# Kernel optimization log

Measured on AMD Instinct MI355X. Metric: run time of the kernel, lower is better.

The kernel has to match this reference:

```python
import jax, jax.numpy as jnp
import numpy as np

N_HEAD = 16

def setup_inputs() -> dict:
    key = jax.random.key(0)
    ks = jax.random.split(key, 5)
    C = 1024
    x = jax.random.normal(ks[0], (2, 2048, C), dtype=jnp.float32)
    W_qkv = jax.random.normal(ks[1], (C, 3 * C), dtype=jnp.float32) * (C ** -0.5)
    b_qkv = jnp.zeros((3 * C,), dtype=jnp.float32)
    W_proj = jax.random.normal(ks[2], (C, C), dtype=jnp.float32) * (C ** -0.5)
    b_proj = jnp.zeros((C,), dtype=jnp.float32)
    return {"x": x, "W_qkv": W_qkv, "b_qkv": b_qkv, "W_proj": W_proj, "b_proj": b_proj}

def reference(x, W_qkv, b_qkv, W_proj, b_proj):
    B, T, C = x.shape
    H = N_HEAD
    D = C // H
    scale = D ** -0.5
    qkv = x @ W_qkv + b_qkv                      # [B,T,3C]
    q, k, v = jnp.split(qkv, 3, axis=-1)
    # [B,T,C] -> [B,H,T,D]
    q = q.reshape(B, T, H, D).transpose(0, 2, 1, 3)
    k = k.reshape(B, T, H, D).transpose(0, 2, 1, 3)
    v = v.reshape(B, T, H, D).transpose(0, 2, 1, 3)
    attn = jnp.einsum('bhqd,bhkd->bhqk', q, k) * scale   # [B,H,T,T]
    causal = jnp.tril(jnp.ones((T, T), dtype=bool))
    attn = jnp.where(causal, attn, -jnp.inf)
    attn = jax.nn.softmax(attn, axis=-1)
    y = jnp.einsum('bhqk,bhkd->bhqd', attn, v)           # [B,H,T,D]
    y = y.transpose(0, 2, 1, 3).reshape(B, T, C)
    return y @ W_proj + b_proj
```

## Files before the change

### kernel.cpp

```cpp
#include <hip/hip_runtime.h>

typedef __attribute__((ext_vector_type(8))) _Float16 h8;
typedef __attribute__((ext_vector_type(4))) _Float16 h4;
typedef __attribute__((ext_vector_type(4))) float f4;

#define QKSCALE 0.18033688011112042f

__device__ __forceinline__ void gload16(const void* g, void* l) {
  __builtin_amdgcn_global_load_lds((const __attribute__((address_space(1))) void*)g,
                                   (__attribute__((address_space(3))) void*)l, 16, 0, 0);
}

__global__ __launch_bounds__(256) void cast_f16_kernel(const float* __restrict__ in,
                                                       _Float16* __restrict__ out, int n) {
  int i = (blockIdx.x * 256 + threadIdx.x) * 8;
  if (i >= n) return;
  const float4* p = (const float4*)(in + i);
  float4 a = p[0], b = p[1];
  h8 v;
  v[0] = (_Float16)a.x; v[1] = (_Float16)a.y; v[2] = (_Float16)a.z; v[3] = (_Float16)a.w;
  v[4] = (_Float16)b.x; v[5] = (_Float16)b.y; v[6] = (_Float16)b.z; v[7] = (_Float16)b.w;
  *(h8*)(out + i) = v;
}

__global__ __launch_bounds__(256) void transp_cast_kernel(const float* __restrict__ W,
                                                          _Float16* __restrict__ Wt, int K, int N) {
  __shared__ _Float16 tile[64][72];
  int k0 = blockIdx.y * 64, n0 = blockIdx.x * 64;
  int t = threadIdx.x;
#pragma unroll
  for (int i = 0; i < 16; ++i) {
    int idx = i * 256 + t;
    int kr = idx >> 6, nc = idx & 63;
    tile[kr][nc] = (_Float16)W[(size_t)(k0 + kr) * N + n0 + nc];
  }
  __syncthreads();
#pragma unroll
  for (int i = 0; i < 2; ++i) {
    int idx = i * 256 + t;
    int nr = idx >> 3, kc = (idx & 7) * 8;
    h8 v;
#pragma unroll
    for (int j = 0; j < 8; ++j) v[j] = tile[kc + j][nr];
    *(h8*)&Wt[(size_t)(n0 + nr) * K + k0 + kc] = v;
  }
}

template <int MODE>
__global__ __launch_bounds__(256) void gemm_f16(const _Float16* __restrict__ A,
                                                const _Float16* __restrict__ Bt,
                                                const float* __restrict__ bias,
                                                float* __restrict__ outF,
                                                _Float16* __restrict__ oQ,
                                                _Float16* __restrict__ oK,
                                                _Float16* __restrict__ oV,
                                                int M, int N, int K) {
  __shared__ _Float16 As[128 * 64];
  __shared__ _Float16 Bs[128 * 64];
  const int m0 = blockIdx.y * 128, n0 = blockIdx.x * 128;
  const int tid = threadIdx.x;
  const int wave = tid >> 6, lane = tid & 63;
  const int wr = (wave >> 1) * 64, wc = (wave & 1) * 64;
  const int lrow = lane & 15, g = lane >> 4;

  const int row_ = tid >> 3, c_ = tid & 7;

  f4 acc[4][4];
  const f4 z4 = {0.f, 0.f, 0.f, 0.f};
#pragma unroll
  for (int m = 0; m < 4; ++m)
#pragma unroll
    for (int n = 0; n < 4; ++n) acc[m][n] = z4;

  for (int k0 = 0; k0 < K; k0 += 64) {
#pragma unroll
    for (int i = 0; i < 4; ++i) {
      int row = i * 32 + row_;
      int cs = (c_ ^ (row & 7)) * 8;
      int ldst = (i * 256 + tid) * 8;
      gload16(&A[(size_t)(m0 + row) * K + k0 + cs], &As[ldst]);
      gload16(&Bt[(size_t)(n0 + row) * K + k0 + cs], &Bs[ldst]);
    }
    __syncthreads();
#pragma unroll
    for (int ss = 0; ss < 2; ++ss) {
      h8 af[4], bf[4];
#pragma unroll
      for (int m = 0; m < 4; ++m) {
        int row = wr + m * 16 + lrow;
        af[m] = *(const h8*)&As[row * 64 + (((ss * 4 + g) ^ (row & 7)) * 8)];
      }
#pragma unroll
      for (int n = 0; n < 4; ++n) {
        int row = wc + n * 16 + lrow;
        bf[n] = *(const h8*)&Bs[row * 64 + (((ss * 4 + g) ^ (row & 7)) * 8)];
      }
      __builtin_amdgcn_s_setprio(1);
#pragma unroll
      for (int m = 0; m < 4; ++m)
#pragma unroll
        for (int n = 0; n < 4; ++n)
          acc[m][n] = __builtin_amdgcn_mfma_f32_16x16x32_f16(af[m], bf[n], acc[m][n], 0, 0, 0);
      __builtin_amdgcn_s_setprio(0);
    }
    __syncthreads();
  }

#pragma unroll
  for (int n = 0; n < 4; ++n) {
    const int gcol = n0 + wc + n * 16 + lrow;
    const float bv = bias ? bias[gcol] : 0.f;
    if (MODE == 1 && (gcol >> 10) == 2) {
      const int c1 = gcol & 1023;
      const int hh = c1 >> 6, d = c1 & 63;
#pragma unroll
      for (int m = 0; m < 4; ++m) {
        const int grow = m0 + wr + m * 16 + g * 4;
        const int b = grow >> 11, t = grow & 2047;
        h4 pv;
#pragma unroll
        for (int r = 0; r < 4; ++r) pv[r] = (_Float16)(acc[m][n][r] + bv);
        *(h4*)&oV[(((size_t)(b * 16 + hh)) * 64 + d) * 2048 + t] = pv;
      }
    } else {
#pragma unroll
      for (int m = 0; m < 4; ++m) {
#pragma unroll
        for (int r = 0; r < 4; ++r) {
          const int grow = m0 + wr + m * 16 + g * 4 + r;
          float v = acc[m][n][r] + bv;
          if (MODE == 0) {
            outF[(size_t)grow * N + gcol] = v;
          } else {
            int part = gcol >> 10;
            int c1 = gcol & 1023;
            int hh = c1 >> 6, d = c1 & 63;
            int b = grow >> 11, t = grow & 2047;
            int bh = b * 16 + hh;
            if (part == 0)
              oQ[((size_t)bh * 2048 + t) * 64 + d] = (_Float16)(v * QKSCALE);
            else
              oK[((size_t)bh * 2048 + t) * 64 + d] = (_Float16)v;
          }
        }
      }
    }
  }
}

__global__ __launch_bounds__(256) void attn_kernel(const _Float16* __restrict__ Qg,
                                                   const _Float16* __restrict__ Kg,
                                                   const _Float16* __restrict__ Vtg,
                                                   _Float16* __restrict__ Og) {
  __shared__ _Float16 slab[4][32][72];
  __shared__ float mlds[2][4][32];

  const int idx = blockIdx.x;
  const int bh = (idx & 7) | (((idx >> 3) & 3) << 3);
  const int pi = idx >> 5;

  const int wave = threadIdx.x >> 6, lane = threadIdx.x & 63;
  const int lrow = lane & 15, g = lane >> 4;
  const int b = bh >> 4, h = bh & 15;
  const _Float16* Q = Qg + (size_t)bh * 2048 * 64;
  const _Float16* K = Kg + (size_t)bh * 2048 * 64;
  const _Float16* Vt = Vtg + (size_t)bh * 64 * 2048;
  _Float16(*pw)[72] = slab[wave];
  const f4 z4 = {0.f, 0.f, 0.f, 0.f};

  for (int half = 0; half < 2; ++half) {
    const int qt2 = half == 0 ? 63 - pi : pi;
    const int q0 = qt2 * 32;

    h8 aq[2][2];
#pragma unroll
    for (int mt = 0; mt < 2; ++mt)
#pragma unroll
      for (int ss = 0; ss < 2; ++ss)
        aq[mt][ss] = *(const h8*)&Q[(q0 + mt * 16 + lrow) * 64 + ss * 32 + g * 8];

    f4 o[2][4];
#pragma unroll
    for (int mt = 0; mt < 2; ++mt)
#pragma unroll
      for (int dt = 0; dt < 4; ++dt) o[mt][dt] = z4;
    float mrow[2][4], lpart[2][4];
#pragma unroll
    for (int mt = 0; mt < 2; ++mt)
#pragma unroll
      for (int r = 0; r < 4; ++r) { mrow[mt][r] = -1e30f; lpart[mt][r] = 0.f; }

    const int NT = (qt2 >> 1) + 1;

    for (int it = wave; it < NT; it += 4) {
      const int kv0 = it * 64;
      h8 kf[4][2];
#pragma unroll
      for (int ct = 0; ct < 4; ++ct)
#pragma unroll
        for (int ss = 0; ss < 2; ++ss)
          kf[ct][ss] = *(const h8*)&K[(kv0 + ct * 16 + lrow) * 64 + ss * 32 + g * 8];

      f4 s[2][4];
#pragma unroll
      for (int mt = 0; mt < 2; ++mt)
#pragma unroll
        for (int ct = 0; ct < 4; ++ct) s[mt][ct] = z4;
#pragma unroll
      for (int ss = 0; ss < 2; ++ss)
#pragma unroll
        for (int mt = 0; mt < 2; ++mt)
#pragma unroll
          for (int ct = 0; ct < 4; ++ct)
            s[mt][ct] = __builtin_amdgcn_mfma_f32_16x16x32_f16(aq[mt][ss], kf[ct][ss], s[mt][ct], 0, 0, 0);

      h8 vf[4][2];
#pragma unroll
      for (int dt = 0; dt < 4; ++dt)
#pragma unroll
        for (int ss = 0; ss < 2; ++ss)
          vf[dt][ss] = *(const h8*)&Vt[(size_t)(dt * 16 + lrow) * 2048 + kv0 + ss * 32 + g * 8];

      if (it == NT - 1) {
#pragma unroll
        for (int mt = 0; mt < 2; ++mt)
#pragma unroll
          for (int ct = 0; ct < 4; ++ct)
#pragma unroll
            for (int r = 0; r < 4; ++r)
              if (kv0 + ct * 16 + lrow > q0 + mt * 16 + g * 4 + r) s[mt][ct][r] = -1e30f;
      }

      float pm[2][4];
      bool need = false;
#pragma unroll
      for (int mt = 0; mt < 2; ++mt)
#pragma unroll
        for (int r = 0; r < 4; ++r) {
          pm[mt][r] = fmaxf(fmaxf(s[mt][0][r], s[mt][1][r]), fmaxf(s[mt][2][r], s[mt][3][r]));
          need = need || (pm[mt][r] > mrow[mt][r] + 8.f);
        }
      if (__any(need)) {
#pragma unroll
        for (int mt = 0; mt < 2; ++mt)
#pragma unroll
          for (int r = 0; r < 4; ++r) {
            float m = pm[mt][r];
            m = fmaxf(m, __shfl_xor(m, 1));
            m = fmaxf(m, __shfl_xor(m, 2));
            m = fmaxf(m, __shfl_xor(m, 4));
            m = fmaxf(m, __shfl_xor(m, 8));
            float mn = fmaxf(mrow[mt][r], m);
            float fr = __builtin_amdgcn_exp2f(mrow[mt][r] - mn);
            mrow[mt][r] = mn;
            lpart[mt][r] *= fr;
#pragma unroll
            for (int dt = 0; dt < 4; ++dt) o[mt][dt][r] *= fr;
          }
      }
#pragma unroll
      for (int mt = 0; mt < 2; ++mt)
#pragma unroll
        for (int r = 0; r < 4; ++r) {
          float ps = 0.f;
#pragma unroll
          for (int ct = 0; ct < 4; ++ct) {
            float p = __builtin_amdgcn_exp2f(s[mt][ct][r] - mrow[mt][r]);
            ps += p;
            pw[mt * 16 + g * 4 + r][ct * 16 + lrow] = (_Float16)p;
          }
          lpart[mt][r] += ps;
        }

      h8 ap[2][2];
#pragma unroll
      for (int mt = 0; mt < 2; ++mt)
#pragma unroll
        for (int ss = 0; ss < 2; ++ss)
          ap[mt][ss] = *(const h8*)&pw[mt * 16 + lrow][ss * 32 + g * 8];

#pragma unroll
      for (int ss = 0; ss < 2; ++ss)
#pragma unroll
        for (int mt = 0; mt < 2; ++mt)
#pragma unroll
          for (int dt = 0; dt < 4; ++dt)
            o[mt][dt] = __builtin_amdgcn_mfma_f32_16x16x32_f16(ap[mt][ss], vf[dt][ss], o[mt][dt], 0, 0, 0);
    }

#pragma unroll
    for (int mt = 0; mt < 2; ++mt)
#pragma unroll
      for (int r = 0; r < 4; ++r) {
        float l = lpart[mt][r];
        l += __shfl_xor(l, 1);
        l += __shfl_xor(l, 2);
        l += __shfl_xor(l, 4);
        l += __shfl_xor(l, 8);
        lpart[mt][r] = l;
      }

    if (lrow == 0) {
#pragma unroll
      for (int mt = 0; mt < 2; ++mt)
#pragma unroll
        for (int r = 0; r < 4; ++r) {
          mlds[0][wave][mt * 16 + g * 4 + r] = mrow[mt][r];
          mlds[1][wave][mt * 16 + g * 4 + r] = lpart[mt][r];
        }
    }
#pragma unroll
    for (int mt = 0; mt < 2; ++mt)
#pragma unroll
      for (int r = 0; r < 4; ++r) {
        float inv = lpart[mt][r] > 0.f ? 1.f / lpart[mt][r] : 0.f;
#pragma unroll
        for (int dt = 0; dt < 4; ++dt)
          pw[mt * 16 + g * 4 + r][dt * 16 + lrow] = (_Float16)(o[mt][dt][r] * inv);
      }
    __syncthreads();

    {
      const int ql = threadIdx.x >> 3;
      const int d0 = (threadIdx.x & 7) * 8;
      float m0 = mlds[0][0][ql], m1 = mlds[0][1][ql], m2 = mlds[0][2][ql], m3 = mlds[0][3][ql];
      float M = fmaxf(fmaxf(m0, m1), fmaxf(m2, m3));
      float f0 = __builtin_amdgcn_exp2f(m0 - M) * mlds[1][0][ql];
      float f1 = __builtin_amdgcn_exp2f(m1 - M) * mlds[1][1][ql];
      float f2 = __builtin_amdgcn_exp2f(m2 - M) * mlds[1][2][ql];
      float f3 = __builtin_amdgcn_exp2f(m3 - M) * mlds[1][3][ql];
      float inv = 1.f / (f0 + f1 + f2 + f3);
      h8 o0 = *(const h8*)&slab[0][ql][d0];
      h8 o1 = *(const h8*)&slab[1][ql][d0];
      h8 o2 = *(const h8*)&slab[2][ql][d0];
      h8 o3 = *(const h8*)&slab[3][ql][d0];
      h8 outv;
#pragma unroll
      for (int j = 0; j < 8; ++j) {
        float v = f0 * (float)o0[j] + f1 * (float)o1[j] + f2 * (float)o2[j] + f3 * (float)o3[j];
        outv[j] = (_Float16)(v * inv);
      }
      *(h8*)&Og[((size_t)b * 2048 + q0 + ql) * 1024 + h * 64 + d0] = outv;
    }
    if (half == 0) __syncthreads();
  }
}

extern "C" void kernel_launch(void* const* d_in, const int* in_sizes, int n_in,
                              void* d_out, int out_size, void* d_ws, size_t ws_size,
                              hipStream_t stream) {
  const float* x = (const float*)d_in[0];
  const float* Wqkv = (const float*)d_in[1];
  const float* bqkv = (const float*)d_in[2];
  const float* Wproj = (const float*)d_in[3];
  const float* bproj = (const float*)d_in[4];
  float* out = (float*)d_out;

  char* ws = (char*)d_ws;
  const size_t MB = 1u << 20;
  _Float16* xh     = (_Float16*)(ws + 0 * MB);
  _Float16* wqkvt  = (_Float16*)(ws + 8 * MB);
  _Float16* wprojt = (_Float16*)(ws + 14 * MB);
  _Float16* qh     = (_Float16*)(ws + 16 * MB);
  _Float16* kh     = (_Float16*)(ws + 24 * MB);
  _Float16* vth    = (_Float16*)(ws + 32 * MB);
  _Float16* oh     = (_Float16*)(ws + 40 * MB);

  cast_f16_kernel<<<2048, 256, 0, stream>>>(x, xh, 4194304);
  transp_cast_kernel<<<dim3(48, 16), 256, 0, stream>>>(Wqkv, wqkvt, 1024, 3072);
  transp_cast_kernel<<<dim3(16, 16), 256, 0, stream>>>(Wproj, wprojt, 1024, 1024);

  gemm_f16<1><<<dim3(24, 32), 256, 0, stream>>>(xh, wqkvt, bqkv, nullptr, qh, kh, vth,
                                                4096, 3072, 1024);
  attn_kernel<<<dim3(1024), 256, 0, stream>>>(qh, kh, vth, oh);
  gemm_f16<0><<<dim3(8, 32), 256, 0, stream>>>(oh, wprojt, bproj, out, nullptr, nullptr, nullptr,
                                               4096, 1024, 1024);
}
```

Baseline: 151.8 us.

## Rewrite attention inner loop with 32x32x16 MFMA and register-resident P

Switches the attention kernel from 16x16x32 MFMA tiles to 32x32x16 tiles and computes S transposed (K as the A operand, Q as B), so each lane owns one query column. Softmax row max and sum then need only a single cross-half shuffle. P is packed to fp16 in registers and rearranged with lane swaps to feed the PV MFMA directly, removing the per-tile LDS write and read of P. s_setprio hints are added around the MFMA blocks. The risks are extra shuffle and select overhead and higher register pressure from the 16-wide accumulators.

Measured after the change: 149.3 us. Within noise of the previous version (-1.6%).

```diff
diff --git a/kernel.cpp b/kernel.cpp
--- a/kernel.cpp
+++ b/kernel.cpp
@@ -2,13 +2,23 @@
 
 typedef __attribute__((ext_vector_type(8))) _Float16 h8;
 typedef __attribute__((ext_vector_type(4))) _Float16 h4;
+typedef __attribute__((ext_vector_type(2))) _Float16 h2;
 typedef __attribute__((ext_vector_type(4))) float f4;
+typedef __attribute__((ext_vector_type(16))) float f16v;
 
 #define QKSCALE 0.18033688011112042f
+#define Z16 {0.f,0.f,0.f,0.f,0.f,0.f,0.f,0.f,0.f,0.f,0.f,0.f,0.f,0.f,0.f,0.f}
 
 __device__ __forceinline__ void gload16(const void* g, void* l) {
   __builtin_amdgcn_global_load_lds((const __attribute__((address_space(1))) void*)g,
                                    (__attribute__((address_space(3))) void*)l, 16, 0, 0);
+}
+
+__device__ __forceinline__ h2 pkh2(float a, float b) {
+  return __builtin_bit_cast(h2, __builtin_amdgcn_cvt_pkrtz(a, b));
+}
+__device__ __forceinline__ h2 swap32_h2(h2 v) {
+  return __builtin_bit_cast(h2, __shfl_xor(__builtin_bit_cast(int, v), 32));
 }
 
 __global__ __launch_bounds__(256) void cast_f16_kernel(const float* __restrict__ in,
@@ -160,164 +170,138 @@
   const int pi = idx >> 5;
 
   const int wave = threadIdx.x >> 6, lane = threadIdx.x & 63;
-  const int lrow = lane & 15, g = lane >> 4;
+  const int ln = lane & 31, hi = lane >> 5;
   const int b = bh >> 4, h = bh & 15;
   const _Float16* Q = Qg + (size_t)bh * 2048 * 64;
   const _Float16* K = Kg + (size_t)bh * 2048 * 64;
   const _Float16* Vt = Vtg + (size_t)bh * 64 * 2048;
   _Float16(*pw)[72] = slab[wave];
-  const f4 z4 = {0.f, 0.f, 0.f, 0.f};
 
   for (int half = 0; half < 2; ++half) {
     const int qt2 = half == 0 ? 63 - pi : pi;
     const int q0 = qt2 * 32;
 
-    h8 aq[2][2];
-#pragma unroll
-    for (int mt = 0; mt < 2; ++mt)
-#pragma unroll
-      for (int ss = 0; ss < 2; ++ss)
-        aq[mt][ss] = *(const h8*)&Q[(q0 + mt * 16 + lrow) * 64 + ss * 32 + g * 8];
-
-    f4 o[2][4];
-#pragma unroll
-    for (int mt = 0; mt < 2; ++mt)
-#pragma unroll
-      for (int dt = 0; dt < 4; ++dt) o[mt][dt] = z4;
-    float mrow[2][4], lpart[2][4];
-#pragma unroll
-    for (int mt = 0; mt < 2; ++mt)
-#pragma unroll
-      for (int r = 0; r < 4; ++r) { mrow[mt][r] = -1e30f; lpart[mt][r] = 0.f; }
-
+    h8 qf[4];
+#pragma unroll
+    for (int ds = 0; ds < 4; ++ds)
+      qf[ds] = *(const h8*)&Q[(q0 + ln) * 64 + ds * 16 + hi * 8];
+
+    f16v o0 = Z16, o1 = Z16;
+    float m = -1e30f, l = 0.f;
     const int NT = (qt2 >> 1) + 1;
 
     for (int it = wave; it < NT; it += 4) {
       const int kv0 = it * 64;
-      h8 kf[4][2];
-#pragma unroll
-      for (int ct = 0; ct < 4; ++ct)
-#pragma unroll
-        for (int ss = 0; ss < 2; ++ss)
-          kf[ct][ss] = *(const h8*)&K[(kv0 + ct * 16 + lrow) * 64 + ss * 32 + g * 8];
-
-      f4 s[2][4];
-#pragma unroll
-      for (int mt = 0; mt < 2; ++mt)
-#pragma unroll
-        for (int ct = 0; ct < 4; ++ct) s[mt][ct] = z4;
-#pragma unroll
-      for (int ss = 0; ss < 2; ++ss)
-#pragma unroll
-        for (int mt = 0; mt < 2; ++mt)
-#pragma unroll
-          for (int ct = 0; ct < 4; ++ct)
-            s[mt][ct] = __builtin_amdgcn_mfma_f32_16x16x32_f16(aq[mt][ss], kf[ct][ss], s[mt][ct], 0, 0, 0);
-
-      h8 vf[4][2];
-#pragma unroll
-      for (int dt = 0; dt < 4; ++dt)
-#pragma unroll
-        for (int ss = 0; ss < 2; ++ss)
-          vf[dt][ss] = *(const h8*)&Vt[(size_t)(dt * 16 + lrow) * 2048 + kv0 + ss * 32 + g * 8];
+      h8 kf[2][4];
+#pragma unroll
+      for (int kt = 0; kt < 2; ++kt)
+#pragma unroll
+        for (int ds = 0; ds < 4; ++ds)
+          kf[kt][ds] = *(const h8*)&K[(kv0 + kt * 32 + ln) * 64 + ds * 16 + hi * 8];
+
+      f16v s0 = Z16, s1 = Z16;
+      __builtin_amdgcn_s_setprio(1);
+#pragma unroll
+      for (int ds = 0; ds < 4; ++ds)
+        s0 = __builtin_amdgcn_mfma_f32_32x32x16_f16(kf[0][ds], qf[ds], s0, 0, 0, 0);
+#pragma unroll
+      for (int ds = 0; ds < 4; ++ds)
+        s1 = __builtin_amdgcn_mfma_f32_32x32x16_f16(kf[1][ds], qf[ds], s1, 0, 0, 0);
+      __builtin_amdgcn_s_setprio(0);
+
+      h8 vf[2][4];
+#pragma unroll
+      for (int dt = 0; dt < 2; ++dt)
+#pragma unroll
+        for (int ks = 0; ks < 4; ++ks)
+          vf[dt][ks] = *(const h8*)&Vt[(size_t)(dt * 32 + ln) * 2048 + kv0 + ks * 16 + hi * 8];
 
       if (it == NT - 1) {
-#pragma unroll
-        for (int mt = 0; mt < 2; ++mt)
-#pragma unroll
-          for (int ct = 0; ct < 4; ++ct)
-#pragma unroll
-            for (int r = 0; r < 4; ++r)
-              if (kv0 + ct * 16 + lrow > q0 + mt * 16 + g * 4 + r) s[mt][ct][r] = -1e30f;
-      }
-
-      float pm[2][4];
-      bool need = false;
-#pragma unroll
-      for (int mt = 0; mt < 2; ++mt)
-#pragma unroll
-        for (int r = 0; r < 4; ++r) {
-          pm[mt][r] = fmaxf(fmaxf(s[mt][0][r], s[mt][1][r]), fmaxf(s[mt][2][r], s[mt][3][r]));
-          need = need || (pm[mt][r] > mrow[mt][r] + 8.f);
+        const int qg = q0 + ln;
+#pragma unroll
+        for (int reg = 0; reg < 16; ++reg) {
+          const int crow = (reg & 3) + 8 * (reg >> 2) + 4 * hi;
+          if (kv0 + crow > qg) s0[reg] = -1e30f;
+          if (kv0 + 32 + crow > qg) s1[reg] = -1e30f;
         }
-      if (__any(need)) {
-#pragma unroll
-        for (int mt = 0; mt < 2; ++mt)
-#pragma unroll
-          for (int r = 0; r < 4; ++r) {
-            float m = pm[mt][r];
-            m = fmaxf(m, __shfl_xor(m, 1));
-            m = fmaxf(m, __shfl_xor(m, 2));
-            m = fmaxf(m, __shfl_xor(m, 4));
-            m = fmaxf(m, __shfl_xor(m, 8));
-            float mn = fmaxf(mrow[mt][r], m);
-            float fr = __builtin_amdgcn_exp2f(mrow[mt][r] - mn);
-            mrow[mt][r] = mn;
-            lpart[mt][r] *= fr;
-#pragma unroll
-            for (int dt = 0; dt < 4; ++dt) o[mt][dt][r] *= fr;
-          }
-      }
-#pragma unroll
-      for (int mt = 0; mt < 2; ++mt)
-#pragma unroll
-        for (int r = 0; r < 4; ++r) {
-          float ps = 0.f;
-#pragma unroll
-          for (int ct = 0; ct < 4; ++ct) {
-            float p = __builtin_amdgcn_exp2f(s[mt][ct][r] - mrow[mt][r]);
-            ps += p;
-            pw[mt * 16 + g * 4 + r][ct * 16 + lrow] = (_Float16)p;
-          }
-          lpart[mt][r] += ps;
+      }
+
+      float pm = fmaxf(s0[0], s1[0]);
+#pragma unroll
+      for (int reg = 1; reg < 16; ++reg) pm = fmaxf(pm, fmaxf(s0[reg], s1[reg]));
+      pm = fmaxf(pm, __shfl_xor(pm, 32));
+
+      if (__any(pm > m + 8.f)) {
+        const float mn = fmaxf(m, pm);
+        const float fr = __builtin_amdgcn_exp2f(m - mn);
+        m = mn;
+        l *= fr;
+#pragma unroll
+        for (int reg = 0; reg < 16; ++reg) {
+          const float frr = __shfl(fr, (reg & 3) + 8 * (reg >> 2) + 4 * hi);
+          o0[reg] *= frr;
+          o1[reg] *= frr;
         }
-
-      h8 ap[2][2];
-#pragma unroll
-      for (int mt = 0; mt < 2; ++mt)
-#pragma unroll
-        for (int ss = 0; ss < 2; ++ss)
-          ap[mt][ss] = *(const h8*)&pw[mt * 16 + lrow][ss * 32 + g * 8];
-
-#pragma unroll
-      for (int ss = 0; ss < 2; ++ss)
-#pragma unroll
-        for (int mt = 0; mt < 2; ++mt)
-#pragma unroll
-          for (int dt = 0; dt < 4; ++dt)
-            o[mt][dt] = __builtin_amdgcn_mfma_f32_16x16x32_f16(ap[mt][ss], vf[dt][ss], o[mt][dt], 0, 0, 0);
-    }
-
-#pragma unroll
-    for (int mt = 0; mt < 2; ++mt)
-#pragma unroll
-      for (int r = 0; r < 4; ++r) {
-        float l = lpart[mt][r];
-        l += __shfl_xor(l, 1);
-        l += __shfl_xor(l, 2);
-        l += __shfl_xor(l, 4);
-        l += __shfl_xor(l, 8);
-        lpart[mt][r] = l;
-      }
-
-    if (lrow == 0) {
-#pragma unroll
-      for (int mt = 0; mt < 2; ++mt)
-#pragma unroll
-        for (int r = 0; r < 4; ++r) {
-          mlds[0][wave][mt * 16 + g * 4 + r] = mrow[mt][r];
-          mlds[1][wave][mt * 16 + g * 4 + r] = lpart[mt][r];
+      }
+
+      float ls = 0.f;
+#pragma unroll
+      for (int reg = 0; reg < 16; ++reg) {
+        s0[reg] = __builtin_amdgcn_exp2f(s0[reg] - m);
+        s1[reg] = __builtin_amdgcn_exp2f(s1[reg] - m);
+        ls += s0[reg] + s1[reg];
+      }
+      l += ls;
+
+      h2 Pk0[4][2], Pk1[4][2];
+#pragma unroll
+      for (int R = 0; R < 4; ++R)
+#pragma unroll
+        for (int pr = 0; pr < 2; ++pr) {
+          Pk0[R][pr] = pkh2(s0[4 * R + 2 * pr], s0[4 * R + 2 * pr + 1]);
+          Pk1[R][pr] = pkh2(s1[4 * R + 2 * pr], s1[4 * R + 2 * pr + 1]);
         }
-    }
-#pragma unroll
-    for (int mt = 0; mt < 2; ++mt)
-#pragma unroll
-      for (int r = 0; r < 4; ++r) {
-        float inv = lpart[mt][r] > 0.f ? 1.f / lpart[mt][r] : 0.f;
-#pragma unroll
-        for (int dt = 0; dt < 4; ++dt)
-          pw[mt * 16 + g * 4 + r][dt * 16 + lrow] = (_Float16)(o[mt][dt][r] * inv);
-      }
+
+      __builtin_amdgcn_s_setprio(1);
+#pragma unroll
+      for (int ks = 0; ks < 4; ++ks) {
+        const int Rb = 2 * (ks & 1);
+        h2 a0p0 = (ks >> 1) ? Pk1[Rb][0] : Pk0[Rb][0];
+        h2 a0p1 = (ks >> 1) ? Pk1[Rb][1] : Pk0[Rb][1];
+        h2 a1p0 = (ks >> 1) ? Pk1[Rb + 1][0] : Pk0[Rb + 1][0];
+        h2 a1p1 = (ks >> 1) ? Pk1[Rb + 1][1] : Pk0[Rb + 1][1];
+        h2 loc0 = hi ? a1p0 : a0p0;
+        h2 loc1 = hi ? a1p1 : a0p1;
+        h2 snd0 = hi ? a0p0 : a1p0;
+        h2 snd1 = hi ? a0p1 : a1p1;
+        h2 rem0 = swap32_h2(snd0);
+        h2 rem1 = swap32_h2(snd1);
+        h2 w0 = hi ? rem0 : loc0;
+        h2 w1 = hi ? rem1 : loc1;
+        h2 w2 = hi ? loc0 : rem0;
+        h2 w3 = hi ? loc1 : rem1;
+        h8 pa;
+        pa[0] = w0[0]; pa[1] = w0[1]; pa[2] = w1[0]; pa[3] = w1[1];
+        pa[4] = w2[0]; pa[5] = w2[1]; pa[6] = w3[0]; pa[7] = w3[1];
+        o0 = __builtin_amdgcn_mfma_f32_32x32x16_f16(pa, vf[0][ks], o0, 0, 0, 0);
+        o1 = __builtin_amdgcn_mfma_f32_32x32x16_f16(pa, vf[1][ks], o1, 0, 0, 0);
+      }
+      __builtin_amdgcn_s_setprio(0);
+    }
+
+    const float l_all = l + __shfl_xor(l, 32);
+    if (hi == 0) {
+      mlds[0][wave][ln] = m;
+      mlds[1][wave][ln] = l_all;
+    }
+#pragma unroll
+    for (int reg = 0; reg < 16; ++reg) {
+      const int crow = (reg & 3) + 8 * (reg >> 2) + 4 * hi;
+      const float li = __shfl(l_all, crow);
+      const float inv = li > 0.f ? 1.f / li : 0.f;
+      pw[crow][ln] = (_Float16)(o0[reg] * inv);
+      pw[crow][32 + ln] = (_Float16)(o1[reg] * inv);
+    }
     __syncthreads();
 
     {
@@ -330,14 +314,14 @@
       float f2 = __builtin_amdgcn_exp2f(m2 - M) * mlds[1][2][ql];
       float f3 = __builtin_amdgcn_exp2f(m3 - M) * mlds[1][3][ql];
       float inv = 1.f / (f0 + f1 + f2 + f3);
-      h8 o0 = *(const h8*)&slab[0][ql][d0];
-      h8 o1 = *(const h8*)&slab[1][ql][d0];
-      h8 o2 = *(const h8*)&slab[2][ql][d0];
-      h8 o3 = *(const h8*)&slab[3][ql][d0];
+      h8 o0v = *(const h8*)&slab[0][ql][d0];
+      h8 o1v = *(const h8*)&slab[1][ql][d0];
+      h8 o2v = *(const h8*)&slab[2][ql][d0];
+      h8 o3v = *(const h8*)&slab[3][ql][d0];
       h8 outv;
 #pragma unroll
       for (int j = 0; j < 8; ++j) {
-        float v = f0 * (float)o0[j] + f1 * (float)o1[j] + f2 * (float)o2[j] + f3 * (float)o3[j];
+        float v = f0 * (float)o0v[j] + f1 * (float)o1v[j] + f2 * (float)o2v[j] + f3 * (float)o3v[j];
         outv[j] = (_Float16)(v * inv);
       }
       *(h8*)&Og[((size_t)b * 2048 + q0 + ql) * 1024 + h * 64 + d0] = outv;
```
